# Performance work log

Measured on AMD Instinct MI355X. Metric: run time of the kernel, lower is better.

## Reference

```python
import jax, jax.numpy as jnp
import numpy as np

N_GRAPHS = 64
NEG_SLOPE = 0.2

def setup_inputs() -> dict:
    key = jax.random.key(0)
    ks = jax.random.split(key, 8)
    N, E, F_IN, H, C, OUT = 50000, 800000, 128, 4, 32, 2
    x = jax.random.normal(ks[0], (N, F_IN), dtype=jnp.float32)
    edge_index = jax.random.randint(ks[1], (2, E), 0, N, dtype=jnp.int64)
    batch = jnp.sort(jax.random.randint(ks[2], (N,), 0, N_GRAPHS, dtype=jnp.int64))
    s = 1.0 / np.sqrt(F_IN)
    W = jax.random.normal(ks[3], (F_IN, H * C), dtype=jnp.float32) * s
    att_src = jax.random.normal(ks[4], (H, C), dtype=jnp.float32) * (1.0 / np.sqrt(C))
    att_dst = jax.random.normal(ks[5], (H, C), dtype=jnp.float32) * (1.0 / np.sqrt(C))
    bias_gat = jnp.zeros((H * C,), dtype=jnp.float32)
    W_lin = jax.random.normal(ks[6], (H * C, OUT), dtype=jnp.float32) * (1.0 / np.sqrt(H * C))
    b_lin = jnp.zeros((OUT,), dtype=jnp.float32)
    return {"x": x, "edge_index": edge_index, "batch": batch, "W": W,
            "att_src": att_src, "att_dst": att_dst, "bias_gat": bias_gat,
            "W_lin": W_lin, "b_lin": b_lin}

def reference(x, edge_index, batch, W, att_src, att_dst, bias_gat, W_lin, b_lin):
    N = x.shape[0]
    H, C = att_src.shape
    # linear projection: [N, H, C]
    xp = (x @ W).reshape(N, H, C)
    # per-node attention logits [N, H]
    a_src = jnp.einsum('nhc,hc->nh', xp, att_src)
    a_dst = jnp.einsum('nhc,hc->nh', xp, att_dst)
    # add self loops (PyG GATConv default add_self_loops=True)
    loop = jnp.arange(N, dtype=edge_index.dtype)
    src = jnp.concatenate([edge_index[0], loop])
    dst = jnp.concatenate([edge_index[1], loop])
    # per-edge logits + leaky relu
    e = a_src[src] + a_dst[dst]                       # [E+N, H]
    e = jnp.where(e >= 0, e, NEG_SLOPE * e)
    # segment softmax over destination node
    emax = jax.ops.segment_max(e, dst, num_segments=N)
    emax = jnp.where(jnp.isfinite(emax), emax, 0.0)
    ee = jnp.exp(e - emax[dst])
    denom = jax.ops.segment_sum(ee, dst, num_segments=N)
    alpha = ee / jnp.maximum(denom[dst], 1e-16)       # [E+N, H]
    # scatter-add aggregation of weighted source features
    msg = alpha[:, :, None] * xp[src]                 # [E+N, H, C]
    out = jax.ops.segment_sum(msg, dst, num_segments=N)  # [N, H, C]
    out = out.reshape(N, H * C) + bias_gat
    out = jax.nn.relu(out)
    # global mean pool per graph
    pooled = jax.ops.segment_sum(out, batch, num_segments=N_GRAPHS)
    counts = jax.ops.segment_sum(jnp.ones((N,), out.dtype), batch, num_segments=N_GRAPHS)
    pooled = pooled / jnp.maximum(counts, 1.0)[:, None]
    return pooled @ W_lin + b_lin
```

## Files before the change

### kernel.cpp

```cpp
#include <hip/hip_runtime.h>
#include <hip/hip_bf16.h>

#define HEADS 4
#define CH    32
#define HC    128
#define FIN   128
#define NG    64
#define POOL_CHUNKS 8
#define CAP   64

typedef __bf16 bf16x8 __attribute__((ext_vector_type(8)));
typedef float  f32x4  __attribute__((ext_vector_type(4)));

__global__ void wtrans_kernel(const float* __restrict__ W,
                              __hip_bfloat16* __restrict__ WT) {
    int t = blockIdx.x * 256 + threadIdx.x;
    if (t < HC * FIN) {
        int n = t >> 7, k = t & 127;
        WT[n * FIN + k] = __float2bfloat16(W[k * HC + n]);
    }
}

__global__ __launch_bounds__(256) void proj_mfma_kernel(const float* __restrict__ x,
                                                        const __hip_bfloat16* __restrict__ WT,
                                                        const float* __restrict__ att_src,
                                                        const float* __restrict__ att_dst,
                                                        __hip_bfloat16* __restrict__ xb,
                                                        float* __restrict__ a_src,
                                                        float* __restrict__ a_dst,
                                                        int N) {
    __shared__ char Xl[64 * 256];
    __shared__ char Wl[128 * 256];
    int t = threadIdx.x;
    int base = blockIdx.x * 64;

    for (int v = t; v < 1024; v += 256) {
        int row = v >> 4, g = v & 15;
        int node = base + row;
        union { bf16x8 v8; uint4 u4; } tmp;
        if (node < N) {
            float4 f0 = *(const float4*)&x[(size_t)node * FIN + g * 8];
            float4 f1 = *(const float4*)&x[(size_t)node * FIN + g * 8 + 4];
            tmp.v8[0] = (__bf16)f0.x; tmp.v8[1] = (__bf16)f0.y;
            tmp.v8[2] = (__bf16)f0.z; tmp.v8[3] = (__bf16)f0.w;
            tmp.v8[4] = (__bf16)f1.x; tmp.v8[5] = (__bf16)f1.y;
            tmp.v8[6] = (__bf16)f1.z; tmp.v8[7] = (__bf16)f1.w;
        } else {
            tmp.u4 = make_uint4(0, 0, 0, 0);
        }
        int gs = g ^ (row & 7);
        *(uint4*)&Xl[row * 256 + gs * 16] = tmp.u4;
    }
    for (int v = t; v < 2048; v += 256) {
        int n = v >> 4, g = v & 15;
        uint4 u = *(const uint4*)&WT[n * FIN + g * 8];
        int gs = g ^ (n & 7);
        *(uint4*)&Wl[n * 256 + gs * 16] = u;
    }
    __syncthreads();

    int wv = t >> 6, lane = t & 63;
    int lr = lane & 15, lg = lane >> 4;
    f32x4 acc[8];
#pragma unroll
    for (int tt = 0; tt < 8; tt++) acc[tt] = (f32x4){0.f, 0.f, 0.f, 0.f};

#pragma unroll
    for (int kc = 0; kc < 4; kc++) {
        int rowl = wv * 16 + lr;
        int ga = (kc * 4 + lg) ^ (lr & 7);
        bf16x8 a = *(bf16x8*)&Xl[rowl * 256 + ga * 16];
#pragma unroll
        for (int tt = 0; tt < 8; tt++) {
            int nr = tt * 16 + lr;
            int gb = (kc * 4 + lg) ^ (lr & 7);
            bf16x8 b = *(bf16x8*)&Wl[nr * 256 + gb * 16];
            acc[tt] = __builtin_amdgcn_mfma_f32_16x16x32_bf16(a, b, acc[tt], 0, 0, 0);
        }
    }

    float ps[4][4];
    float pd[4][4];
#pragma unroll
    for (int r = 0; r < 4; r++)
#pragma unroll
        for (int h = 0; h < 4; h++) { ps[r][h] = 0.f; pd[r][h] = 0.f; }

#pragma unroll
    for (int tt = 0; tt < 8; tt++) {
        int h = tt >> 1;
        int c = (tt & 1) * 16 + lr;
        float sv = att_src[h * CH + c];
        float dv = att_dst[h * CH + c];
        int col = tt * 16 + lr;
#pragma unroll
        for (int r = 0; r < 4; r++) {
            int row = base + wv * 16 + lg * 4 + r;
            float v = acc[tt][r];
            if (row < N) xb[(size_t)row * HC + col] = __float2bfloat16(v);
            ps[r][h] += v * sv;
            pd[r][h] += v * dv;
        }
    }

    __syncthreads();
    float* ssrc = (float*)Wl;
    float* sdst = ((float*)Wl) + 64 * 68;
#pragma unroll
    for (int r = 0; r < 4; r++) {
        int rowl = wv * 16 + lg * 4 + r;
#pragma unroll
        for (int h = 0; h < 4; h++) {
            ssrc[rowl * 68 + lr * 4 + h] = ps[r][h];
            sdst[rowl * 68 + lr * 4 + h] = pd[r][h];
        }
    }
    __syncthreads();
    {
        int rowl = t >> 2, h = t & 3;
        int node = base + rowl;
        float ss = 0.f, sd = 0.f;
#pragma unroll
        for (int q = 0; q < 16; q++) {
            ss += ssrc[rowl * 68 + q * 4 + h];
            sd += sdst[rowl * 68 + q * 4 + h];
        }
        if (node < N) {
            a_src[node * 4 + h] = ss;
            a_dst[node * 4 + h] = sd;
        }
    }
}

__global__ __launch_bounds__(256) void csr_scatter(const int* __restrict__ esrc,
                                                   const int* __restrict__ edst,
                                                   int* __restrict__ cnt,
                                                   int* __restrict__ bucket,
                                                   int E, int EN) {
    int i = blockIdx.x * 256 + threadIdx.x;
    if (i >= EN) return;
    int s, d;
    if (i < E) { s = esrc[i]; d = edst[i]; } else { s = i - E; d = s; }
    int pos = atomicAdd(&cnt[d], 1);
    if (pos < CAP) bucket[(size_t)d * CAP + pos] = s;
}

__global__ __launch_bounds__(256) void agg_csr_kernel(const int* __restrict__ cnt,
                                                      const int* __restrict__ bucket,
                                                      const float* __restrict__ a_src,
                                                      const float* __restrict__ a_dst,
                                                      const __hip_bfloat16* __restrict__ xb,
                                                      float* __restrict__ agg, int N) {
    __shared__ int   ssrc[2][CAP];
    __shared__ float sw[2][CAP * 4];
    __shared__ float srd[2][4];
    int nd = threadIdx.x >> 7;
    int j  = threadIdx.x & 127;
    int d  = blockIdx.x * 2 + nd;
    bool valid = d < N;
    int deg = valid ? min(cnt[d], CAP) : 0;
    const int* lst = bucket + (size_t)d * CAP;

    for (int p = j; p < deg; p += 128) ssrc[nd][p] = lst[p];
    __syncthreads();
    for (int p = j; p < deg * 4; p += 128) {
        int i = p >> 2, h = p & 3;
        int s = ssrc[nd][i];
        float e = a_src[s * 4 + h] + a_dst[d * 4 + h];
        e = e >= 0.f ? e : 0.2f * e;
        sw[nd][p] = __expf(e);
    }
    __syncthreads();
    if (j < 4) {
        float den = 0.f;
        for (int i = 0; i < deg; i++) den += sw[nd][i * 4 + j];
        srd[nd][j] = 1.0f / fmaxf(den, 1e-16f);
    }
    __syncthreads();

    int h = j >> 5;
    float num = 0.f;
    int i = 0;
    for (; i + 4 <= deg; i += 4) {
        int s0 = ssrc[nd][i],     s1 = ssrc[nd][i + 1];
        int s2 = ssrc[nd][i + 2], s3 = ssrc[nd][i + 3];
        float x0 = __bfloat162float(xb[(size_t)s0 * HC + j]);
        float x1 = __bfloat162float(xb[(size_t)s1 * HC + j]);
        float x2 = __bfloat162float(xb[(size_t)s2 * HC + j]);
        float x3 = __bfloat162float(xb[(size_t)s3 * HC + j]);
        float w0 = sw[nd][(i + 0) * 4 + h], w1 = sw[nd][(i + 1) * 4 + h];
        float w2 = sw[nd][(i + 2) * 4 + h], w3 = sw[nd][(i + 3) * 4 + h];
        num += (w0 * x0 + w1 * x1) + (w2 * x2 + w3 * x3);
    }
    for (; i < deg; i++) {
        int s0 = ssrc[nd][i];
        num += sw[nd][i * 4 + h] * __bfloat162float(xb[(size_t)s0 * HC + j]);
    }
    if (valid) agg[(size_t)d * HC + j] = num * srd[nd][h];
}

__global__ __launch_bounds__(256) void pool_kernel(const float* __restrict__ agg,
                                                   const float* __restrict__ bias,
                                                   const int* __restrict__ batch,
                                                   float* __restrict__ pooled,
                                                   float* __restrict__ counts, int N) {
    int g = blockIdx.x / POOL_CHUNKS;
    int chunk = blockIdx.x % POOL_CHUNKS;
    int t = threadIdx.x;

    int lo = 0, hi = N;
    while (lo < hi) { int mid = (lo + hi) >> 1; if (batch[mid] < g) lo = mid + 1; else hi = mid; }
    int gstart = lo;
    hi = N;
    while (lo < hi) { int mid = (lo + hi) >> 1; if (batch[mid] < g + 1) lo = mid + 1; else hi = mid; }
    int gend = lo;
    int cnt = gend - gstart;

    int per = (cnt + POOL_CHUNKS - 1) / POOL_CHUNKS;
    int cstart = gstart + chunk * per;
    int cend = min(cstart + per, gend);

    int col = t & 31;
    int row = t >> 5;
    float4 b4 = *(const float4*)&bias[col * 4];
    float4 acc = make_float4(0.f, 0.f, 0.f, 0.f);
    for (int n = cstart + row; n < cend; n += 8) {
        float4 v = *(const float4*)&agg[(size_t)n * HC + col * 4];
        acc.x += fmaxf(v.x + b4.x, 0.f);
        acc.y += fmaxf(v.y + b4.y, 0.f);
        acc.z += fmaxf(v.z + b4.z, 0.f);
        acc.w += fmaxf(v.w + b4.w, 0.f);
    }

    __shared__ float4 red[256];
    red[t] = acc;
    __syncthreads();
    if (t < 128) {
        red[t].x += red[t + 128].x; red[t].y += red[t + 128].y;
        red[t].z += red[t + 128].z; red[t].w += red[t + 128].w;
    }
    __syncthreads();
    if (t < 64) {
        red[t].x += red[t + 64].x; red[t].y += red[t + 64].y;
        red[t].z += red[t + 64].z; red[t].w += red[t + 64].w;
    }
    __syncthreads();
    if (t < 32) {
        float4 r = red[t];
        r.x += red[t + 32].x; r.y += red[t + 32].y;
        r.z += red[t + 32].z; r.w += red[t + 32].w;
        atomicAdd(&pooled[g * HC + t * 4 + 0], r.x);
        atomicAdd(&pooled[g * HC + t * 4 + 1], r.y);
        atomicAdd(&pooled[g * HC + t * 4 + 2], r.z);
        atomicAdd(&pooled[g * HC + t * 4 + 3], r.w);
    }
    if (t == 0 && chunk == 0) counts[g] = (float)cnt;
}

__global__ void final_kernel(const float* __restrict__ pooled,
                             const float* __restrict__ counts,
                             const float* __restrict__ W_lin,
                             const float* __restrict__ b_lin,
                             float* __restrict__ out) {
    int t = threadIdx.x;
    int g = t >> 1, o = t & 1;
    float cnt = fmaxf(counts[g], 1.f);
    float sum = 0.f;
#pragma unroll 8
    for (int k = 0; k < HC; k++) sum += pooled[g * HC + k] * W_lin[k * 2 + o];
    out[g * 2 + o] = sum / cnt + b_lin[o];
}

extern "C" void kernel_launch(void* const* d_in, const int* in_sizes, int n_in,
                              void* d_out, int out_size, void* d_ws, size_t ws_size,
                              hipStream_t stream) {
    const float* x       = (const float*)d_in[0];
    const int*   eidx    = (const int*)d_in[1];
    const int*   batch   = (const int*)d_in[2];
    const float* W       = (const float*)d_in[3];
    const float* att_src = (const float*)d_in[4];
    const float* att_dst = (const float*)d_in[5];
    const float* bias    = (const float*)d_in[6];
    const float* W_lin   = (const float*)d_in[7];
    const float* b_lin   = (const float*)d_in[8];
    float* out = (float*)d_out;

    int N  = in_sizes[0] / FIN;
    int E  = in_sizes[1] / 2;
    int EN = E + N;
    const int* esrc = eidx;
    const int* edst = eidx + E;

    char* wsb = (char*)d_ws;
    __hip_bfloat16* xb = (__hip_bfloat16*)wsb; wsb += (size_t)N * HC * 2;
    float* a_src  = (float*)wsb;          wsb += (size_t)N * 4 * 4;
    float* a_dst  = (float*)wsb;          wsb += (size_t)N * 4 * 4;
    float* agg    = (float*)wsb;          wsb += (size_t)N * HC * 4;
    float* pooled = (float*)wsb;          wsb += (size_t)NG * HC * 4;
    float* counts = (float*)wsb;          wsb += (size_t)NG * 4;
    int*   cnt    = (int*)wsb;            wsb += (size_t)N * 4;
    int*   bucket = (int*)wsb;            wsb += (size_t)N * CAP * 4;
    __hip_bfloat16* WT = (__hip_bfloat16*)wsb; wsb += (size_t)HC * FIN * 2;

    hipMemsetAsync(cnt, 0, (size_t)N * sizeof(int), stream);
    hipMemsetAsync(pooled, 0, (size_t)(NG * HC + NG) * sizeof(float), stream);

    wtrans_kernel<<<(HC * FIN + 255) / 256, 256, 0, stream>>>(W, WT);
    proj_mfma_kernel<<<(N + 63) / 64, 256, 0, stream>>>(x, WT, att_src, att_dst,
                                                        xb, a_src, a_dst, N);
    csr_scatter<<<(EN + 255) / 256, 256, 0, stream>>>(esrc, edst, cnt, bucket, E, EN);
    agg_csr_kernel<<<(N + 1) / 2, 256, 0, stream>>>(cnt, bucket, a_src, a_dst, xb, agg, N);
    pool_kernel<<<NG * POOL_CHUNKS, 256, 0, stream>>>(agg, bias, batch, pooled, counts, N);
    final_kernel<<<1, 128, 0, stream>>>(pooled, counts, W_lin, b_lin, out);
}
```

Measured before the change: 229.9 us.

## Assign one wavefront per destination node in aggregation, dropping block barriers

Rewrites the aggregation kernel so each 64-lane wavefront handles one destination node instead of 128 threads per node. Block-wide barriers give way to wave-local shared memory plus shuffle reductions for the softmax denominators. Each lane now loads two bf16 features as one 32-bit word and writes a float2, halving the number of gather instructions. There is no barrier between the shared-memory writes of the source ids and weights and the reads by other lanes; this relies on lockstep wavefront execution and could be fragile.

```diff
diff --git a/kernel.cpp b/kernel.cpp
--- a/kernel.cpp
+++ b/kernel.cpp
@@ -145,58 +145,66 @@
     if (pos < CAP) bucket[(size_t)d * CAP + pos] = s;
 }
 
-__global__ __launch_bounds__(256) void agg_csr_kernel(const int* __restrict__ cnt,
-                                                      const int* __restrict__ bucket,
-                                                      const float* __restrict__ a_src,
-                                                      const float* __restrict__ a_dst,
-                                                      const __hip_bfloat16* __restrict__ xb,
-                                                      float* __restrict__ agg, int N) {
-    __shared__ int   ssrc[2][CAP];
-    __shared__ float sw[2][CAP * 4];
-    __shared__ float srd[2][4];
-    int nd = threadIdx.x >> 7;
-    int j  = threadIdx.x & 127;
-    int d  = blockIdx.x * 2 + nd;
-    bool valid = d < N;
-    int deg = valid ? min(cnt[d], CAP) : 0;
+__global__ __launch_bounds__(256) void agg_wave_kernel(const int* __restrict__ cnt,
+                                                       const int* __restrict__ bucket,
+                                                       const float* __restrict__ a_src,
+                                                       const float* __restrict__ a_dst,
+                                                       const __hip_bfloat16* __restrict__ xb,
+                                                       float* __restrict__ agg, int N) {
+    __shared__ int   sid[4][CAP];
+    __shared__ float sw[4][CAP * 4];
+    int wv = threadIdx.x >> 6;
+    int lane = threadIdx.x & 63;
+    int d = blockIdx.x * 4 + wv;
+    if (d >= N) return;
+    int deg = min(cnt[d], CAP);
     const int* lst = bucket + (size_t)d * CAP;
 
-    for (int p = j; p < deg; p += 128) ssrc[nd][p] = lst[p];
-    __syncthreads();
-    for (int p = j; p < deg * 4; p += 128) {
-        int i = p >> 2, h = p & 3;
-        int s = ssrc[nd][i];
-        float e = a_src[s * 4 + h] + a_dst[d * 4 + h];
+    if (lane < deg) sid[wv][lane] = lst[lane];
+
+    float adh = a_dst[d * 4 + (lane & 3)];
+    float wpart = 0.f;
+    for (int p = lane; p < deg * 4; p += 64) {
+        int i = p >> 2;
+        int s = sid[wv][i];
+        float e = a_src[s * 4 + (lane & 3)] + adh;
         e = e >= 0.f ? e : 0.2f * e;
-        sw[nd][p] = __expf(e);
-    }
-    __syncthreads();
-    if (j < 4) {
-        float den = 0.f;
-        for (int i = 0; i < deg; i++) den += sw[nd][i * 4 + j];
-        srd[nd][j] = 1.0f / fmaxf(den, 1e-16f);
-    }
-    __syncthreads();
-
-    int h = j >> 5;
-    float num = 0.f;
+        float w = __expf(e);
+        sw[wv][p] = w;
+        wpart += w;
+    }
+#pragma unroll
+    for (int off = 4; off < 64; off <<= 1) wpart += __shfl_xor(wpart, off, 64);
+    float rdc = 1.0f / fmaxf(wpart, 1e-16f);
+    int h = lane >> 4;
+    float rd = __shfl(rdc, h, 64);
+
+    int j0 = lane * 2;
+    float n0 = 0.f, n1 = 0.f;
     int i = 0;
     for (; i + 4 <= deg; i += 4) {
-        int s0 = ssrc[nd][i],     s1 = ssrc[nd][i + 1];
-        int s2 = ssrc[nd][i + 2], s3 = ssrc[nd][i + 3];
-        float x0 = __bfloat162float(xb[(size_t)s0 * HC + j]);
-        float x1 = __bfloat162float(xb[(size_t)s1 * HC + j]);
-        float x2 = __bfloat162float(xb[(size_t)s2 * HC + j]);
-        float x3 = __bfloat162float(xb[(size_t)s3 * HC + j]);
-        float w0 = sw[nd][(i + 0) * 4 + h], w1 = sw[nd][(i + 1) * 4 + h];
-        float w2 = sw[nd][(i + 2) * 4 + h], w3 = sw[nd][(i + 3) * 4 + h];
-        num += (w0 * x0 + w1 * x1) + (w2 * x2 + w3 * x3);
+        int s0 = sid[wv][i], s1 = sid[wv][i + 1];
+        int s2 = sid[wv][i + 2], s3 = sid[wv][i + 3];
+        unsigned u0 = *(const unsigned*)&xb[(size_t)s0 * HC + j0];
+        unsigned u1 = *(const unsigned*)&xb[(size_t)s1 * HC + j0];
+        unsigned u2 = *(const unsigned*)&xb[(size_t)s2 * HC + j0];
+        unsigned u3 = *(const unsigned*)&xb[(size_t)s3 * HC + j0];
+        float w0 = sw[wv][(i + 0) * 4 + h], w1 = sw[wv][(i + 1) * 4 + h];
+        float w2 = sw[wv][(i + 2) * 4 + h], w3 = sw[wv][(i + 3) * 4 + h];
+        n0 += w0 * __uint_as_float(u0 << 16) + w1 * __uint_as_float(u1 << 16)
+            + w2 * __uint_as_float(u2 << 16) + w3 * __uint_as_float(u3 << 16);
+        n1 += w0 * __uint_as_float(u0 & 0xffff0000u) + w1 * __uint_as_float(u1 & 0xffff0000u)
+            + w2 * __uint_as_float(u2 & 0xffff0000u) + w3 * __uint_as_float(u3 & 0xffff0000u);
     }
     for (; i < deg; i++) {
-        int s0 = ssrc[nd][i];
-        num += sw[nd][i * 4 + h] * __bfloat162float(xb[(size_t)s0 * HC + j]);
-    }
-    if (valid) agg[(size_t)d * HC + j] = num * srd[nd][h];
+        int s0 = sid[wv][i];
+        unsigned u0 = *(const unsigned*)&xb[(size_t)s0 * HC + j0];
+        float w0 = sw[wv][i * 4 + h];
+        n0 += w0 * __uint_as_float(u0 << 16);
+        n1 += w0 * __uint_as_float(u0 & 0xffff0000u);
+    }
+    float2 o = make_float2(n0 * rd, n1 * rd);
+    *(float2*)&agg[(size_t)d * HC + j0] = o;
 }
 
 __global__ __launch_bounds__(256) void pool_kernel(const float* __restrict__ agg,
@@ -309,7 +317,7 @@
     proj_mfma_kernel<<<(N + 63) / 64, 256, 0, stream>>>(x, WT, att_src, att_dst,
                                                         xb, a_src, a_dst, N);
     csr_scatter<<<(EN + 255) / 256, 256, 0, stream>>>(esrc, edst, cnt, bucket, E, EN);
-    agg_csr_kernel<<<(N + 1) / 2, 256, 0, stream>>>(cnt, bucket, a_src, a_dst, xb, agg, N);
+    agg_wave_kernel<<<(N + 3) / 4, 256, 0, stream>>>(cnt, bucket, a_src, a_dst, xb, agg, N);
     pool_kernel<<<NG * POOL_CHUNKS, 256, 0, stream>>>(agg, bias, batch, pooled, counts, N);
     final_kernel<<<1, 128, 0, stream>>>(pooled, counts, W_lin, b_lin, out);
 }
```

New measurement: 213.9 us. -7.0%, faster.
